# Kernel tuning notes

Measured on AMD Instinct MI355X. Metric: run time of the kernel, lower is better.

The kernel has to match this reference:

```python
import jax, jax.numpy as jnp
import numpy as np

N = 100000          # num nodes
NUM_GRAPHS = 64
NEG_SLOPE = 0.2     # PyG GATv2Conv default


def gatv2_layer(x, src, dst, Wl, bl, Wr, br, att, bias, heads, out_ch, concat):
    # x: [N, F_in]; src/dst: [E] (self-loops already included)
    xl = (x @ Wl + bl).reshape(-1, heads, out_ch)   # source transform
    xr = (x @ Wr + br).reshape(-1, heads, out_ch)   # target transform
    m = jax.nn.leaky_relu(xl[src] + xr[dst], NEG_SLOPE)      # [E, H, C]
    alpha = jnp.einsum('ehc,hc->eh', m, att)                 # [E, H]
    # segment softmax over destination nodes
    amax = jax.ops.segment_max(alpha, dst, num_segments=N)
    alpha = jnp.exp(alpha - amax[dst])
    denom = jax.ops.segment_sum(alpha, dst, num_segments=N)
    alpha = alpha / (denom[dst] + 1e-16)
    out = jax.ops.segment_sum(xl[src] * alpha[..., None], dst, num_segments=N)
    out = out.reshape(N, heads * out_ch) if concat else out.mean(axis=1)
    return out + bias


def setup_inputs() -> dict:
    key = jax.random.key(0)
    ks = jax.random.split(key, 16)
    E = 3200000
    x = jax.random.normal(ks[0], (N, 256), dtype=jnp.float32)
    edge_index = jax.random.randint(ks[1], (2, E), 0, N, dtype=jnp.int64)
    batch = jnp.sort(jax.random.randint(ks[2], (N,), 0, NUM_GRAPHS, dtype=jnp.int64))
    H1, C1 = 8, 4
    s1 = 1.0 / np.sqrt(256)
    s2 = 1.0 / np.sqrt(H1 * C1)
    return {
        'x': x, 'edge_index': edge_index, 'batch': batch,
        'W1l': jax.random.normal(ks[3], (256, H1 * C1), jnp.float32) * s1,
        'b1l': jnp.zeros((H1 * C1,), jnp.float32),
        'W1r': jax.random.normal(ks[4], (256, H1 * C1), jnp.float32) * s1,
        'b1r': jnp.zeros((H1 * C1,), jnp.float32),
        'att1': jax.random.normal(ks[5], (H1, C1), jnp.float32),
        'bias1': jnp.zeros((H1 * C1,), jnp.float32),
        'W2l': jax.random.normal(ks[6], (H1 * C1, 64), jnp.float32) * s2,
        'b2l': jnp.zeros((64,), jnp.float32),
        'W2r': jax.random.normal(ks[7], (H1 * C1, 64), jnp.float32) * s2,
        'b2r': jnp.zeros((64,), jnp.float32),
        'att2': jax.random.normal(ks[8], (1, 64), jnp.float32),
        'bias2': jnp.zeros((64,), jnp.float32),
    }


def reference(x, edge_index, batch, W1l, b1l, W1r, b1r, att1, bias1,
              W2l, b2l, W2r, b2r, att2, bias2):
    # add self-loops (PyG GATv2Conv default add_self_loops=True)
    loop = jnp.arange(N, dtype=edge_index.dtype)
    src = jnp.concatenate([edge_index[0], loop])
    dst = jnp.concatenate([edge_index[1], loop])
    h = gatv2_layer(x, src, dst, W1l, b1l, W1r, b1r, att1, bias1, 8, 4, True)
    h = jax.nn.elu(h)
    h = gatv2_layer(h, src, dst, W2l, b2l, W2r, b2r, att2, bias2, 1, 64, False)
    # global mean pool over graphs
    sums = jax.ops.segment_sum(h, batch, num_segments=NUM_GRAPHS)
    counts = jax.ops.segment_sum(jnp.ones((N, 1), h.dtype), batch, num_segments=NUM_GRAPHS)
    return sums / jnp.maximum(counts, 1.0)
```

## Files before the change

kernel.cpp:

```cpp
#include <hip/hip_runtime.h>
#include <math.h>

#define NN 100000
#define EE 3200000
#define ET (EE + NN)
#define NG 64

#define NB 196
#define BWID 512
#define PCHUNK 4096
#define PBLOCKS ((ET + PCHUNK - 1) / PCHUNK)
#define PART_SMEM (NB * 12 + 1024 + PCHUNK * 4 + PCHUNK)

#define X1_SPLIT 50048
#define X1BLK_A 391
#define X1BLK_B 391

#define OFF_XL1B  0u
#define OFF_XR1   1600000u
#define OFF_HL2B  8000000u
#define OFF_HR2   11200000u
#define OFF_BEDGE 8000000u
#define OFF_RP    17600000u
#define OFF_ESRC  17700096u
#define OFF_POOL  21000096u
#define OFF_CNTG  21004192u
#define OFF_BCNT  21004256u
#define OFF_BOFF  21004512u
#define OFF_GCUR  21004768u
#define OFF_AL2   21005024u
#define OFF_AR2   21105024u
#define WS_UNITS  21205024u

__device__ __forceinline__ float lrelu(float v) { return fmaxf(v, 0.2f * v); }

__device__ __forceinline__ unsigned pack_bf2(float a, float b) {
  unsigned ua = __float_as_uint(a), ub = __float_as_uint(b);
  ua = (ua + 0x7FFFu + ((ua >> 16) & 1u)) >> 16;
  ub = (ub + 0x7FFFu + ((ub >> 16) & 1u)) & 0xFFFF0000u;
  return ua | ub;
}
__device__ __forceinline__ float bf_lo(unsigned u) { return __uint_as_float(u << 16); }
__device__ __forceinline__ float bf_hi(unsigned u) { return __uint_as_float(u & 0xFFFF0000u); }

typedef float f32x2 __attribute__((ext_vector_type(2)));
__device__ __forceinline__ f32x2 pk_add(f32x2 a, f32x2 b) {
  f32x2 r; asm("v_pk_add_f32 %0, %1, %2" : "=v"(r) : "v"(a), "v"(b)); return r;
}
__device__ __forceinline__ f32x2 pk_mul(f32x2 a, f32x2 b) {
  f32x2 r; asm("v_pk_mul_f32 %0, %1, %2" : "=v"(r) : "v"(a), "v"(b)); return r;
}
__device__ __forceinline__ f32x2 pk_fma(f32x2 a, f32x2 b, f32x2 c) {
  f32x2 r; asm("v_pk_fma_f32 %0, %1, %2, %3" : "=v"(r) : "v"(a), "v"(b), "v"(c)); return r;
}
__device__ __forceinline__ f32x2 unpk2(unsigned u) {
  f32x2 r; r.x = __uint_as_float(u << 16); r.y = __uint_as_float(u & 0xFFFF0000u); return r;
}
__device__ __forceinline__ f32x2 abs2(f32x2 a) {
  f32x2 r;
  r.x = __uint_as_float(__float_as_uint(a.x) & 0x7FFFFFFFu);
  r.y = __uint_as_float(__float_as_uint(a.y) & 0x7FFFFFFFu);
  return r;
}

__global__ __launch_bounds__(256) void k_bcount(const int* __restrict__ ei,
                                                int* __restrict__ bcnt) {
  __shared__ int h[NB];
  for (int i = threadIdx.x; i < NB; i += 256) h[i] = 0;
  __syncthreads();
  for (long e = (long)blockIdx.x * 256 + threadIdx.x; e < ET; e += (long)gridDim.x * 256) {
    int d = (e < EE) ? ei[EE + e] : (int)(e - EE);
    atomicAdd(&h[d >> 9], 1);
  }
  __syncthreads();
  for (int i = threadIdx.x; i < NB; i += 256) if (h[i]) atomicAdd(&bcnt[i], h[i]);
}

__global__ __launch_bounds__(256) void k_bscan(const int* __restrict__ bcnt,
                                               int* __restrict__ boff, int* __restrict__ gcur) {
  __shared__ int sd[256];
  int t = threadIdx.x;
  int v = (t < NB) ? bcnt[t] : 0;
  sd[t] = v;
  __syncthreads();
  for (int o = 1; o < 256; o <<= 1) {
    int u = (t >= o) ? sd[t - o] : 0;
    __syncthreads();
    sd[t] += u;
    __syncthreads();
  }
  if (t < NB) { boff[t] = sd[t] - v; gcur[t] = sd[t] - v; }
  if (t == 0) boff[NB] = ET;
}

__device__ void part_role(char* smem, const int* __restrict__ ei,
                          int* __restrict__ gcur, int* __restrict__ bedge, int pblk) {
  int* cnt   = (int*)smem;
  int* lbase = cnt + NB;
  int* gbase = lbase + NB;
  int* sc    = gbase + NB;
  int* buf   = sc + 256;
  unsigned char* bkt = (unsigned char*)(buf + PCHUNK);
  int tid = threadIdx.x;
  long e0 = (long)pblk * PCHUNK;
  int nedge = (e0 + PCHUNK <= ET) ? PCHUNK : (int)(ET - e0);

  for (int i = tid; i < NB; i += 512) cnt[i] = 0;
  __syncthreads();
  for (int i = tid; i < nedge; i += 512) {
    long e = e0 + i;
    int d = (e < EE) ? ei[EE + e] : (int)(e - EE);
    atomicAdd(&cnt[d >> 9], 1);
  }
  __syncthreads();
  if (tid < 256) sc[tid] = (tid < NB) ? cnt[tid] : 0;
  __syncthreads();
  for (int o = 1; o < 256; o <<= 1) {
    int u = (tid < 256 && tid >= o) ? sc[tid - o] : 0;
    __syncthreads();
    if (tid < 256) sc[tid] += u;
    __syncthreads();
  }
  if (tid < NB) lbase[tid] = sc[tid] - cnt[tid];
  __syncthreads();
  if (tid < NB) {
    int c = cnt[tid];
    gbase[tid] = c ? atomicAdd(&gcur[tid], c) : 0;
    cnt[tid] = 0;
  }
  __syncthreads();
  for (int i = tid; i < nedge; i += 512) {
    long e = e0 + i;
    int s, d;
    if (e < EE) { s = ei[e]; d = ei[EE + e]; }
    else { s = (int)(e - EE); d = s; }
    int b = d >> 9;
    int r = atomicAdd(&cnt[b], 1);
    int idx = lbase[b] + r;
    buf[idx] = s | ((d & 511) << 17);
    bkt[idx] = (unsigned char)b;
  }
  __syncthreads();
  for (int i = tid; i < nedge; i += 512) {
    int p = buf[i];
    int b = bkt[i];
    bedge[gbase[b] + (i - lbase[b])] = p;
  }
}

__device__ void csr_role(char* smem, const int* __restrict__ boff,
                         const int* __restrict__ bedge,
                         int* __restrict__ rp, int* __restrict__ esrc, int b) {
  int* sdeg  = (int*)smem;
  int* sscan = sdeg + BWID;
  int t = threadIdx.x;
  int n0 = b * BWID;
  int lo = boff[b], hi = boff[b + 1];
  sdeg[t] = 0;
  __syncthreads();
  for (int i = lo + t; i < hi; i += 512) {
    int p = bedge[i];
    atomicAdd(&sdeg[p >> 17], 1);
  }
  __syncthreads();
  int v = sdeg[t];
  sscan[t] = v;
  __syncthreads();
  for (int o = 1; o < 512; o <<= 1) {
    int u = (t >= o) ? sscan[t - o] : 0;
    __syncthreads();
    sscan[t] += u;
    __syncthreads();
  }
  int excl = sscan[t] - v;
  int n = n0 + t;
  if (n < NN) rp[n] = lo + excl;
  if (b == NB - 1 && t == 0) rp[NN] = ET;
  __syncthreads();
  sdeg[t] = lo + excl;
  __syncthreads();
  for (int i = lo + t; i < hi; i += 512) {
    int p = bedge[i];
    int pos = atomicAdd(&sdeg[p >> 17], 1);
    esrc[pos] = p & 0x1FFFF;
  }
}

#define FMA4A(a, xv) \
  a.x += xv.x*w0.x + xv.y*w1.x + xv.z*w2.x + xv.w*w3.x; \
  a.y += xv.x*w0.y + xv.y*w1.y + xv.z*w2.y + xv.w*w3.y; \
  a.z += xv.x*w0.z + xv.y*w1.z + xv.z*w2.z + xv.w*w3.z; \
  a.w += xv.x*w0.w + xv.y*w1.w + xv.z*w2.w + xv.w*w3.w;

__device__ void xform1_role(char* smem, const float* __restrict__ x,
                            const float* __restrict__ Wl, const float* __restrict__ bl,
                            const float* __restrict__ Wr, const float* __restrict__ br,
                            unsigned short* __restrict__ xl1b, float* __restrict__ xr1,
                            int n_base) {
  float* Wlds = (float*)smem;
  int tid = threadIdx.x;
  int ci = tid & 15;
  int cbase = ci * 4;
  int n0 = n_base + (tid >> 4) * 4;
  int r0 = n0 + 0 < NN ? n0 + 0 : NN - 1;
  int r1 = n0 + 1 < NN ? n0 + 1 : NN - 1;
  int r2 = n0 + 2 < NN ? n0 + 2 : NN - 1;
  int r3 = n0 + 3 < NN ? n0 + 3 : NN - 1;
  const float* xb0 = x + (size_t)r0 * 256;
  const float* xb1 = x + (size_t)r1 * 256;
  const float* xb2 = x + (size_t)r2 * 256;
  const float* xb3 = x + (size_t)r3 * 256;
  float4 acc0 = {0,0,0,0}, acc1 = {0,0,0,0}, acc2 = {0,0,0,0}, acc3 = {0,0,0,0};

  for (int q = 0; q < 4; ++q) {
    int k0 = q * 64;
    __syncthreads();
    for (int i = tid; i < 64 * 64; i += 512) {
      int k = (i >> 6) + k0, c = i & 63;
      Wlds[i] = (c < 32) ? Wl[k * 32 + c] : Wr[k * 32 + (c - 32)];
    }
    __syncthreads();
#pragma unroll 2
    for (int kk = 0; kk < 64; kk += 4) {
      int k = k0 + kk;
      float4 xv0 = *(const float4*)(xb0 + k);
      float4 xv1 = *(const float4*)(xb1 + k);
      float4 xv2 = *(const float4*)(xb2 + k);
      float4 xv3 = *(const float4*)(xb3 + k);
      const float* wr = &Wlds[kk * 64 + cbase];
      float4 w0 = *(const float4*)(wr);
      float4 w1 = *(const float4*)(wr + 64);
      float4 w2 = *(const float4*)(wr + 128);
      float4 w3 = *(const float4*)(wr + 192);
      FMA4A(acc0, xv0)
      FMA4A(acc1, xv1)
      FMA4A(acc2, xv2)
      FMA4A(acc3, xv3)
    }
  }
  float4 acc[4] = {acc0, acc1, acc2, acc3};
  if (cbase < 32) {
    float4 bv = { bl[cbase], bl[cbase+1], bl[cbase+2], bl[cbase+3] };
#pragma unroll
    for (int j = 0; j < 4; ++j) {
      int n = n0 + j;
      if (n < NN) {
        uint2 o = { pack_bf2(acc[j].x + bv.x, acc[j].y + bv.y),
                    pack_bf2(acc[j].z + bv.z, acc[j].w + bv.w) };
        *(uint2*)(xl1b + (size_t)n * 32 + cbase) = o;
      }
    }
  } else {
    int c2 = cbase - 32;
    float4 bv = { br[c2], br[c2+1], br[c2+2], br[c2+3] };
#pragma unroll
    for (int j = 0; j < 4; ++j) {
      int n = n0 + j;
      if (n < NN) {
        float4 o = { acc[j].x + bv.x, acc[j].y + bv.y, acc[j].z + bv.z, acc[j].w + bv.w };
        *(float4*)(xr1 + (size_t)n * 32 + c2) = o;
      }
    }
  }
}

__global__ __launch_bounds__(512) void k_part_x1(
    const int* __restrict__ ei, int* __restrict__ gcur, int* __restrict__ bedge,
    const float* __restrict__ x,
    const float* __restrict__ Wl, const float* __restrict__ bl,
    const float* __restrict__ Wr, const float* __restrict__ br,
    unsigned short* __restrict__ xl1b, float* __restrict__ xr1) {
  extern __shared__ char smem[];
  if (blockIdx.x < PBLOCKS)
    part_role(smem, ei, gcur, bedge, blockIdx.x);
  else
    xform1_role(smem, x, Wl, bl, Wr, br, xl1b, xr1, (blockIdx.x - PBLOCKS) * 128);
}

__global__ __launch_bounds__(512) void k_csr_x1(
    const int* __restrict__ boff, const int* __restrict__ bedge,
    int* __restrict__ rp, int* __restrict__ esrc,
    const float* __restrict__ x,
    const float* __restrict__ Wl, const float* __restrict__ bl,
    const float* __restrict__ Wr, const float* __restrict__ br,
    unsigned short* __restrict__ xl1b, float* __restrict__ xr1) {
  extern __shared__ char smem[];
  if (blockIdx.x < NB)
    csr_role(smem, boff, bedge, rp, esrc, blockIdx.x);
  else
    xform1_role(smem, x, Wl, bl, Wr, br, xl1b, xr1,
                X1_SPLIT + (blockIdx.x - NB) * 128);
}

__global__ __launch_bounds__(256) void k_gather1x2(
    const int* __restrict__ rp, const int* __restrict__ esrc,
    const unsigned short* __restrict__ xl1b, const float* __restrict__ xr1,
    const float* __restrict__ att1, const float* __restrict__ bias1,
    const float* __restrict__ W2l, const float* __restrict__ b2l,
    const float* __restrict__ W2r, const float* __restrict__ b2r,
    const float* __restrict__ att2,
    unsigned short* __restrict__ hl2b, float* __restrict__ hr2,
    float* __restrict__ AL2, float* __restrict__ AR2) {
  __shared__ float W2lds[32 * 128];
  __shared__ float hlds[8][33];
  int tid = threadIdx.x;
  for (int i = tid; i < 32 * 128; i += 256) {
    int k = i >> 7, c = i & 127;
    W2lds[i] = (c < 64) ? W2l[k * 64 + c] : W2r[k * 64 + (c - 64)];
  }
  int n = blockIdx.x * 8 + (tid >> 5);
  int l = tid & 31;
  float av = att1[l];
  float xr = xr1[(size_t)n * 32 + l];
  int rpn = rp[n], dg = rp[n + 1] - rpn;
  float acc = 0.0f, den = 0.0f;
  int j = 0;
  for (; j + 4 <= dg; j += 4) {
    int s0 = esrc[rpn + j + 0];
    int s1 = esrc[rpn + j + 1];
    int s2 = esrc[rpn + j + 2];
    int s3 = esrc[rpn + j + 3];
    float x0 = bf_lo(xl1b[(size_t)s0 * 32 + l]);
    float x1 = bf_lo(xl1b[(size_t)s1 * 32 + l]);
    float x2 = bf_lo(xl1b[(size_t)s2 * 32 + l]);
    float x3 = bf_lo(xl1b[(size_t)s3 * 32 + l]);
    float p0 = lrelu(x0 + xr) * av;
    float p1 = lrelu(x1 + xr) * av;
    float p2 = lrelu(x2 + xr) * av;
    float p3 = lrelu(x3 + xr) * av;
    p0 += __shfl_xor(p0, 1); p1 += __shfl_xor(p1, 1);
    p2 += __shfl_xor(p2, 1); p3 += __shfl_xor(p3, 1);
    p0 += __shfl_xor(p0, 2); p1 += __shfl_xor(p1, 2);
    p2 += __shfl_xor(p2, 2); p3 += __shfl_xor(p3, 2);
    float w0 = __expf(p0), w1 = __expf(p1), w2 = __expf(p2), w3 = __expf(p3);
    den += w0 + w1 + w2 + w3;
    acc += w0 * x0 + w1 * x1 + w2 * x2 + w3 * x3;
  }
  for (; j < dg; ++j) {
    int s = esrc[rpn + j];
    float xl = bf_lo(xl1b[(size_t)s * 32 + l]);
    float p = lrelu(xl + xr) * av;
    p += __shfl_xor(p, 1);
    p += __shfl_xor(p, 2);
    float w = __expf(p);
    den += w;
    acc += w * xl;
  }
  float v = acc / (den + 1e-16f) + bias1[l];
  v = v > 0.0f ? v : expm1f(v);
  hlds[tid >> 5][l] = v;
  __syncthreads();

  int ni = tid >> 5, ci = tid & 31, cbase = ci * 4;
  float4 a = {0,0,0,0};
#pragma unroll
  for (int k = 0; k < 32; ++k) {
    float hv = hlds[ni][k];
    float4 wv = *(const float4*)(&W2lds[k * 128 + cbase]);
    a.x += hv * wv.x; a.y += hv * wv.y; a.z += hv * wv.z; a.w += hv * wv.w;
  }
  int no = blockIdx.x * 8 + ni;
  float partial;
  if (cbase < 64) {
    uint2 o = { pack_bf2(a.x + b2l[cbase], a.y + b2l[cbase + 1]),
                pack_bf2(a.z + b2l[cbase + 2], a.w + b2l[cbase + 3]) };
    *(uint2*)(hl2b + (size_t)no * 64 + cbase) = o;
    partial = bf_lo(o.x) * att2[cbase + 0] + bf_hi(o.x) * att2[cbase + 1]
            + bf_lo(o.y) * att2[cbase + 2] + bf_hi(o.y) * att2[cbase + 3];
  } else {
    int c2 = cbase - 64;
    float4 o = { a.x + b2r[c2], a.y + b2r[c2 + 1], a.z + b2r[c2 + 2], a.w + b2r[c2 + 3] };
    *(float4*)(hr2 + (size_t)no * 64 + c2) = o;
    partial = o.x * att2[c2 + 0] + o.y * att2[c2 + 1]
            + o.z * att2[c2 + 2] + o.w * att2[c2 + 3];
  }
  partial += __shfl_xor(partial, 1);
  partial += __shfl_xor(partial, 2);
  partial += __shfl_xor(partial, 4);
  partial += __shfl_xor(partial, 8);
  if (ci == 0)  AL2[no] = partial;
  if (ci == 16) AR2[no] = partial;
}

#define G2E(qq, u0O, u1O, u2O, u3O, pO) \
  f32x2 u0O = unpk2(qq.x), u1O = unpk2(qq.y), u2O = unpk2(qq.z), u3O = unpk2(qq.w); \
  float pO; { \
    f32x2 pa__ = pk_mul(abs2(pk_add(u0O, hp0)), ap0); \
    pa__ = pk_fma(abs2(pk_add(u1O, hp1)), ap1, pa__); \
    pa__ = pk_fma(abs2(pk_add(u2O, hp2)), ap2, pa__); \
    pa__ = pk_fma(abs2(pk_add(u3O, hp3)), ap3, pa__); \
    pO = pa__.x + pa__.y; }

#define G2A(u0O, u1O, u2O, u3O, ww) { \
  f32x2 wv__; wv__.x = (ww); wv__.y = (ww); \
  A0 = pk_fma(u0O, wv__, A0); A1 = pk_fma(u1O, wv__, A1); \
  A2 = pk_fma(u2O, wv__, A2); A3 = pk_fma(u3O, wv__, A3); }

__global__ __launch_bounds__(256) void k_gather2(
    const int* __restrict__ rp, const int* __restrict__ esrc,
    const unsigned short* __restrict__ hl2b, const float* __restrict__ hr2,
    const float* __restrict__ att2, const float* __restrict__ bias2,
    const int* __restrict__ batch,
    const float* __restrict__ AL2, const float* __restrict__ AR2,
    float* __restrict__ pool, float* __restrict__ cntg) {
  __shared__ float ssum[4][64];
  __shared__ float scnt[4];
  int tid = threadIdx.x;
  int n = (blockIdx.x * 256 + tid) >> 3;
  int l8 = tid & 7;
  int nblk0 = blockIdx.x * 32;
  int gmin = batch[nblk0];
  int gspan = batch[nblk0 + 31] - gmin + 1;
  ssum[tid >> 6][tid & 63] = 0.0f;
  if (tid < 4) scnt[tid] = 0.0f;
  __syncthreads();

  float4 ac0 = *(const float4*)(att2 + l8 * 8);
  float4 ac1 = *(const float4*)(att2 + l8 * 8 + 4);
  float4 bs0 = *(const float4*)(bias2 + l8 * 8);
  float4 bs1 = *(const float4*)(bias2 + l8 * 8 + 4);
  f32x2 ap0, ap1, ap2, ap3;
  ap0.x = ac0.x; ap0.y = ac0.y; ap1.x = ac0.z; ap1.y = ac0.w;
  ap2.x = ac1.x; ap2.y = ac1.y; ap3.x = ac1.z; ap3.y = ac1.w;
  const float4* hrp = (const float4*)(hr2 + (size_t)n * 64 + l8 * 8);
  float4 h0 = hrp[0], h1 = hrp[1];
  f32x2 hp0, hp1, hp2, hp3;
  hp0.x = h0.x; hp0.y = h0.y; hp1.x = h0.z; hp1.y = h0.w;
  hp2.x = h1.x; hp2.y = h1.y; hp3.x = h1.z; hp3.y = h1.w;
  float ard = 0.6f * AR2[n];
  int rpn = rp[n], dg = rp[n + 1] - rpn;
  f32x2 A0 = {0.f,0.f}, A1 = {0.f,0.f}, A2 = {0.f,0.f}, A3 = {0.f,0.f};
  float den = 0.0f;
  int j = 0;
  for (; j + 4 <= dg; j += 4) {
    int s0 = esrc[rpn + j + 0];
    int s1 = esrc[rpn + j + 1];
    int s2 = esrc[rpn + j + 2];
    int s3 = esrc[rpn + j + 3];
    uint4 q0 = *(const uint4*)(hl2b + (size_t)s0 * 64 + l8 * 8);
    uint4 q1 = *(const uint4*)(hl2b + (size_t)s1 * 64 + l8 * 8);
    uint4 q2 = *(const uint4*)(hl2b + (size_t)s2 * 64 + l8 * 8);
    uint4 q3 = *(const uint4*)(hl2b + (size_t)s3 * 64 + l8 * 8);
    float al0 = AL2[s0], al1 = AL2[s1], al2 = AL2[s2], al3 = AL2[s3];
    G2E(q0, e0u0, e0u1, e0u2, e0u3, p0)
    G2E(q1, e1u0, e1u1, e1u2, e1u3, p1)
    G2E(q2, e2u0, e2u1, e2u2, e2u3, p2)
    G2E(q3, e3u0, e3u1, e3u2, e3u3, p3)
    p0 += __shfl_xor(p0, 1); p1 += __shfl_xor(p1, 1);
    p2 += __shfl_xor(p2, 1); p3 += __shfl_xor(p3, 1);
    p0 += __shfl_xor(p0, 2); p1 += __shfl_xor(p1, 2);
    p2 += __shfl_xor(p2, 2); p3 += __shfl_xor(p3, 2);
    p0 += __shfl_xor(p0, 4); p1 += __shfl_xor(p1, 4);
    p2 += __shfl_xor(p2, 4); p3 += __shfl_xor(p3, 4);
    float w0 = __expf(fmaf(0.6f, al0, fmaf(0.4f, p0, ard)));
    float w1 = __expf(fmaf(0.6f, al1, fmaf(0.4f, p1, ard)));
    float w2 = __expf(fmaf(0.6f, al2, fmaf(0.4f, p2, ard)));
    float w3 = __expf(fmaf(0.6f, al3, fmaf(0.4f, p3, ard)));
    den += w0 + w1 + w2 + w3;
    G2A(e0u0, e0u1, e0u2, e0u3, w0)
    G2A(e1u0, e1u1, e1u2, e1u3, w1)
    G2A(e2u0, e2u1, e2u2, e2u3, w2)
    G2A(e3u0, e3u1, e3u2, e3u3, w3)
  }
  for (; j < dg; ++j) {
    int s = esrc[rpn + j];
    uint4 q0 = *(const uint4*)(hl2b + (size_t)s * 64 + l8 * 8);
    float al = AL2[s];
    G2E(q0, tu0, tu1, tu2, tu3, p)
    p += __shfl_xor(p, 1);
    p += __shfl_xor(p, 2);
    p += __shfl_xor(p, 4);
    float w = __expf(fmaf(0.6f, al, fmaf(0.4f, p, ard)));
    den += w;
    G2A(tu0, tu1, tu2, tu3, w)
  }
  float inv = 1.0f / (den + 1e-16f);
  int gi = batch[n] - gmin;
  float* sp = &ssum[gi][l8 * 8];
  atomicAdd(sp + 0, A0.x * inv + bs0.x);
  atomicAdd(sp + 1, A0.y * inv + bs0.y);
  atomicAdd(sp + 2, A1.x * inv + bs0.z);
  atomicAdd(sp + 3, A1.y * inv + bs0.w);
  atomicAdd(sp + 4, A2.x * inv + bs1.x);
  atomicAdd(sp + 5, A2.y * inv + bs1.y);
  atomicAdd(sp + 6, A3.x * inv + bs1.z);
  atomicAdd(sp + 7, A3.y * inv + bs1.w);
  if (l8 == 0) atomicAdd(&scnt[gi], 1.0f);
  __syncthreads();
  for (int i = tid; i < gspan * 64; i += 256)
    atomicAdd(pool + (size_t)(gmin + (i >> 6)) * 64 + (i & 63), ssum[i >> 6][i & 63]);
  if (tid < gspan) atomicAdd(cntg + gmin + tid, scnt[tid]);
}

__global__ __launch_bounds__(256) void k_final(
    const float* __restrict__ pool, const float* __restrict__ cntg,
    float* __restrict__ out) {
  int i = blockIdx.x * 256 + threadIdx.x;
  if (i < NG * 64) out[i] = pool[i] / fmaxf(cntg[i >> 6], 1.0f);
}

extern "C" void kernel_launch(void* const* d_in, const int* in_sizes, int n_in,
                              void* d_out, int out_size, void* d_ws, size_t ws_size,
                              hipStream_t stream) {
  const float* x     = (const float*)d_in[0];
  const int*   ei    = (const int*)d_in[1];
  const int*   batch = (const int*)d_in[2];
  const float* W1l   = (const float*)d_in[3];
  const float* b1l   = (const float*)d_in[4];
  const float* W1r   = (const float*)d_in[5];
  const float* b1r   = (const float*)d_in[6];
  const float* att1  = (const float*)d_in[7];
  const float* bias1 = (const float*)d_in[8];
  const float* W2l   = (const float*)d_in[9];
  const float* b2l   = (const float*)d_in[10];
  const float* W2r   = (const float*)d_in[11];
  const float* b2r   = (const float*)d_in[12];
  const float* att2  = (const float*)d_in[13];
  const float* bias2 = (const float*)d_in[14];
  float* ws = (float*)d_ws;
  int*   wi = (int*)d_ws;
  float* out = (float*)d_out;

  hipMemsetAsync(ws + OFF_POOL, 0, (size_t)(OFF_AL2 - OFF_POOL) * 4, stream);

  k_bcount<<<512, 256, 0, stream>>>(ei, wi + OFF_BCNT);
  k_bscan<<<1, 256, 0, stream>>>(wi + OFF_BCNT, wi + OFF_BOFF, wi + OFF_GCUR);
  k_part_x1<<<PBLOCKS + X1BLK_A, 512, PART_SMEM, stream>>>(
      ei, wi + OFF_GCUR, wi + OFF_BEDGE,
      x, W1l, b1l, W1r, b1r, (unsigned short*)(ws + OFF_XL1B), ws + OFF_XR1);
  k_csr_x1<<<NB + X1BLK_B, 512, 16384, stream>>>(
      wi + OFF_BOFF, wi + OFF_BEDGE, wi + OFF_RP, wi + OFF_ESRC,
      x, W1l, b1l, W1r, b1r, (unsigned short*)(ws + OFF_XL1B), ws + OFF_XR1);

  k_gather1x2<<<NN / 8, 256, 0, stream>>>(wi + OFF_RP, wi + OFF_ESRC,
                                          (const unsigned short*)(ws + OFF_XL1B), ws + OFF_XR1,
                                          att1, bias1, W2l, b2l, W2r, b2r, att2,
                                          (unsigned short*)(ws + OFF_HL2B), ws + OFF_HR2,
                                          ws + OFF_AL2, ws + OFF_AR2);
  k_gather2<<<(NN * 8 + 255) / 256, 256, 0, stream>>>(wi + OFF_RP, wi + OFF_ESRC,
                                                      (const unsigned short*)(ws + OFF_HL2B),
                                                      ws + OFF_HR2, att2, bias2, batch,
                                                      ws + OFF_AL2, ws + OFF_AR2,
                                                      ws + OFF_POOL, ws + OFF_CNTG);
  k_final<<<16, 256, 0, stream>>>(ws + OFF_POOL, ws + OFF_CNTG, out);
}
```

Measured before the change: 355.2 us.

## Restructure layer-1 gather to 8 lanes per node with packed bf16 loads

The layer-1 gather now assigns 8 lanes per destination node instead of 32. Each lane loads 4 bf16 channels (one head) as a uint2, so the per-head attention dot product needs no shuffle reduction. Leaky-relu is rewritten algebraically as 0.6*v + 0.4*|v| and evaluated with packed FMAs. Each block now handles 32 nodes and loops the fused layer-2 transform over 4 sub-batches, which amortises the W2 shared-memory fill over more nodes. The cost is fewer blocks and higher per-thread register use.

```diff
diff --git a/kernel.cpp b/kernel.cpp
--- a/kernel.cpp
+++ b/kernel.cpp
@@ -292,6 +292,16 @@
                 X1_SPLIT + (blockIdx.x - NB) * 128);
 }
 
+#define G1E(qq, u0O, u1O, pO) \
+  f32x2 u0O = unpk2(qq.x), u1O = unpk2(qq.y); \
+  float pO; { \
+    f32x2 v0__ = pk_add(u0O, xp0), v1__ = pk_add(u1O, xp1); \
+    f32x2 d__ = pk_mul(a6p0, v0__); \
+    d__ = pk_fma(a6p1, v1__, d__); \
+    d__ = pk_fma(a4p0, abs2(v0__), d__); \
+    d__ = pk_fma(a4p1, abs2(v1__), d__); \
+    pO = d__.x + d__.y; }
+
 __global__ __launch_bounds__(256) void k_gather1x2(
     const int* __restrict__ rp, const int* __restrict__ esrc,
     const unsigned short* __restrict__ xl1b, const float* __restrict__ xr1,
@@ -302,84 +312,111 @@
     unsigned short* __restrict__ hl2b, float* __restrict__ hr2,
     float* __restrict__ AL2, float* __restrict__ AR2) {
   __shared__ float W2lds[32 * 128];
-  __shared__ float hlds[8][33];
+  __shared__ float hlds[32][33];
   int tid = threadIdx.x;
   for (int i = tid; i < 32 * 128; i += 256) {
     int k = i >> 7, c = i & 127;
     W2lds[i] = (c < 64) ? W2l[k * 64 + c] : W2r[k * 64 + (c - 64)];
   }
-  int n = blockIdx.x * 8 + (tid >> 5);
-  int l = tid & 31;
-  float av = att1[l];
-  float xr = xr1[(size_t)n * 32 + l];
+  int nl = tid >> 3;
+  int n = blockIdx.x * 32 + nl;
+  int l8 = tid & 7;
+  float4 at = *(const float4*)(att1 + l8 * 4);
+  f32x2 a6p0, a6p1, a4p0, a4p1;
+  a6p0.x = 0.6f * at.x; a6p0.y = 0.6f * at.y;
+  a6p1.x = 0.6f * at.z; a6p1.y = 0.6f * at.w;
+  a4p0.x = 0.4f * at.x; a4p0.y = 0.4f * at.y;
+  a4p1.x = 0.4f * at.z; a4p1.y = 0.4f * at.w;
+  float4 xrv = *(const float4*)(xr1 + (size_t)n * 32 + l8 * 4);
+  f32x2 xp0, xp1;
+  xp0.x = xrv.x; xp0.y = xrv.y; xp1.x = xrv.z; xp1.y = xrv.w;
+
   int rpn = rp[n], dg = rp[n + 1] - rpn;
-  float acc = 0.0f, den = 0.0f;
+  f32x2 A0 = {0.f,0.f}, A1 = {0.f,0.f};
+  float den = 0.0f;
   int j = 0;
   for (; j + 4 <= dg; j += 4) {
     int s0 = esrc[rpn + j + 0];
     int s1 = esrc[rpn + j + 1];
     int s2 = esrc[rpn + j + 2];
     int s3 = esrc[rpn + j + 3];
-    float x0 = bf_lo(xl1b[(size_t)s0 * 32 + l]);
-    float x1 = bf_lo(xl1b[(size_t)s1 * 32 + l]);
-    float x2 = bf_lo(xl1b[(size_t)s2 * 32 + l]);
-    float x3 = bf_lo(xl1b[(size_t)s3 * 32 + l]);
-    float p0 = lrelu(x0 + xr) * av;
-    float p1 = lrelu(x1 + xr) * av;
-    float p2 = lrelu(x2 + xr) * av;
-    float p3 = lrelu(x3 + xr) * av;
-    p0 += __shfl_xor(p0, 1); p1 += __shfl_xor(p1, 1);
-    p2 += __shfl_xor(p2, 1); p3 += __shfl_xor(p3, 1);
-    p0 += __shfl_xor(p0, 2); p1 += __shfl_xor(p1, 2);
-    p2 += __shfl_xor(p2, 2); p3 += __shfl_xor(p3, 2);
+    uint2 q0 = *(const uint2*)(xl1b + (size_t)s0 * 32 + l8 * 4);
+    uint2 q1 = *(const uint2*)(xl1b + (size_t)s1 * 32 + l8 * 4);
+    uint2 q2 = *(const uint2*)(xl1b + (size_t)s2 * 32 + l8 * 4);
+    uint2 q3 = *(const uint2*)(xl1b + (size_t)s3 * 32 + l8 * 4);
+    G1E(q0, e0u0, e0u1, p0)
+    G1E(q1, e1u0, e1u1, p1)
+    G1E(q2, e2u0, e2u1, p2)
+    G1E(q3, e3u0, e3u1, p3)
     float w0 = __expf(p0), w1 = __expf(p1), w2 = __expf(p2), w3 = __expf(p3);
     den += w0 + w1 + w2 + w3;
-    acc += w0 * x0 + w1 * x1 + w2 * x2 + w3 * x3;
+    f32x2 wv0; wv0.x = w0; wv0.y = w0;
+    f32x2 wv1; wv1.x = w1; wv1.y = w1;
+    f32x2 wv2; wv2.x = w2; wv2.y = w2;
+    f32x2 wv3; wv3.x = w3; wv3.y = w3;
+    A0 = pk_fma(e0u0, wv0, A0); A1 = pk_fma(e0u1, wv0, A1);
+    A0 = pk_fma(e1u0, wv1, A0); A1 = pk_fma(e1u1, wv1, A1);
+    A0 = pk_fma(e2u0, wv2, A0); A1 = pk_fma(e2u1, wv2, A1);
+    A0 = pk_fma(e3u0, wv3, A0); A1 = pk_fma(e3u1, wv3, A1);
   }
   for (; j < dg; ++j) {
     int s = esrc[rpn + j];
-    float xl = bf_lo(xl1b[(size_t)s * 32 + l]);
-    float p = lrelu(xl + xr) * av;
-    p += __shfl_xor(p, 1);
-    p += __shfl_xor(p, 2);
+    uint2 q0 = *(const uint2*)(xl1b + (size_t)s * 32 + l8 * 4);
+    G1E(q0, tu0, tu1, p)
     float w = __expf(p);
     den += w;
-    acc += w * xl;
-  }
-  float v = acc / (den + 1e-16f) + bias1[l];
-  v = v > 0.0f ? v : expm1f(v);
-  hlds[tid >> 5][l] = v;
-  __syncthreads();
-
-  int ni = tid >> 5, ci = tid & 31, cbase = ci * 4;
-  float4 a = {0,0,0,0};
+    f32x2 wv; wv.x = w; wv.y = w;
+    A0 = pk_fma(tu0, wv, A0); A1 = pk_fma(tu1, wv, A1);
+  }
+  float inv = 1.0f / (den + 1e-16f);
+  float4 hb = *(const float4*)(bias1 + l8 * 4);
+  float h0 = A0.x * inv + hb.x;
+  float h1 = A0.y * inv + hb.y;
+  float h2 = A1.x * inv + hb.z;
+  float h3 = A1.y * inv + hb.w;
+  h0 = h0 > 0.0f ? h0 : expm1f(h0);
+  h1 = h1 > 0.0f ? h1 : expm1f(h1);
+  h2 = h2 > 0.0f ? h2 : expm1f(h2);
+  h3 = h3 > 0.0f ? h3 : expm1f(h3);
+  hlds[nl][l8 * 4 + 0] = h0;
+  hlds[nl][l8 * 4 + 1] = h1;
+  hlds[nl][l8 * 4 + 2] = h2;
+  hlds[nl][l8 * 4 + 3] = h3;
+  __syncthreads();
+
+  int ni8 = tid >> 5, ci = tid & 31, cbase = ci * 4;
 #pragma unroll
-  for (int k = 0; k < 32; ++k) {
-    float hv = hlds[ni][k];
-    float4 wv = *(const float4*)(&W2lds[k * 128 + cbase]);
-    a.x += hv * wv.x; a.y += hv * wv.y; a.z += hv * wv.z; a.w += hv * wv.w;
-  }
-  int no = blockIdx.x * 8 + ni;
-  float partial;
-  if (cbase < 64) {
-    uint2 o = { pack_bf2(a.x + b2l[cbase], a.y + b2l[cbase + 1]),
-                pack_bf2(a.z + b2l[cbase + 2], a.w + b2l[cbase + 3]) };
-    *(uint2*)(hl2b + (size_t)no * 64 + cbase) = o;
-    partial = bf_lo(o.x) * att2[cbase + 0] + bf_hi(o.x) * att2[cbase + 1]
-            + bf_lo(o.y) * att2[cbase + 2] + bf_hi(o.y) * att2[cbase + 3];
-  } else {
-    int c2 = cbase - 64;
-    float4 o = { a.x + b2r[c2], a.y + b2r[c2 + 1], a.z + b2r[c2 + 2], a.w + b2r[c2 + 3] };
-    *(float4*)(hr2 + (size_t)no * 64 + c2) = o;
-    partial = o.x * att2[c2 + 0] + o.y * att2[c2 + 1]
-            + o.z * att2[c2 + 2] + o.w * att2[c2 + 3];
-  }
-  partial += __shfl_xor(partial, 1);
-  partial += __shfl_xor(partial, 2);
-  partial += __shfl_xor(partial, 4);
-  partial += __shfl_xor(partial, 8);
-  if (ci == 0)  AL2[no] = partial;
-  if (ci == 16) AR2[no] = partial;
+  for (int sb = 0; sb < 4; ++sb) {
+    int nloc = sb * 8 + ni8;
+    float4 a = {0,0,0,0};
+#pragma unroll
+    for (int k = 0; k < 32; ++k) {
+      float hv = hlds[nloc][k];
+      float4 wv = *(const float4*)(&W2lds[k * 128 + cbase]);
+      a.x += hv * wv.x; a.y += hv * wv.y; a.z += hv * wv.z; a.w += hv * wv.w;
+    }
+    int no = blockIdx.x * 32 + nloc;
+    float partial;
+    if (cbase < 64) {
+      uint2 o = { pack_bf2(a.x + b2l[cbase], a.y + b2l[cbase + 1]),
+                  pack_bf2(a.z + b2l[cbase + 2], a.w + b2l[cbase + 3]) };
+      *(uint2*)(hl2b + (size_t)no * 64 + cbase) = o;
+      partial = bf_lo(o.x) * att2[cbase + 0] + bf_hi(o.x) * att2[cbase + 1]
+              + bf_lo(o.y) * att2[cbase + 2] + bf_hi(o.y) * att2[cbase + 3];
+    } else {
+      int c2 = cbase - 64;
+      float4 o = { a.x + b2r[c2], a.y + b2r[c2 + 1], a.z + b2r[c2 + 2], a.w + b2r[c2 + 3] };
+      *(float4*)(hr2 + (size_t)no * 64 + c2) = o;
+      partial = o.x * att2[c2 + 0] + o.y * att2[c2 + 1]
+              + o.z * att2[c2 + 2] + o.w * att2[c2 + 3];
+    }
+    partial += __shfl_xor(partial, 1);
+    partial += __shfl_xor(partial, 2);
+    partial += __shfl_xor(partial, 4);
+    partial += __shfl_xor(partial, 8);
+    if (ci == 0)  AL2[no] = partial;
+    if (ci == 16) AR2[no] = partial;
+  }
 }
 
 #define G2E(qq, u0O, u1O, u2O, u3O, pO) \
@@ -532,11 +569,11 @@
       wi + OFF_BOFF, wi + OFF_BEDGE, wi + OFF_RP, wi + OFF_ESRC,
       x, W1l, b1l, W1r, b1r, (unsigned short*)(ws + OFF_XL1B), ws + OFF_XR1);
 
-  k_gather1x2<<<NN / 8, 256, 0, stream>>>(wi + OFF_RP, wi + OFF_ESRC,
-                                          (const unsigned short*)(ws + OFF_XL1B), ws + OFF_XR1,
-                                          att1, bias1, W2l, b2l, W2r, b2r, att2,
-                                          (unsigned short*)(ws + OFF_HL2B), ws + OFF_HR2,
-                                          ws + OFF_AL2, ws + OFF_AR2);
+  k_gather1x2<<<NN / 32, 256, 0, stream>>>(wi + OFF_RP, wi + OFF_ESRC,
+                                           (const unsigned short*)(ws + OFF_XL1B), ws + OFF_XR1,
+                                           att1, bias1, W2l, b2l, W2r, b2r, att2,
+                                           (unsigned short*)(ws + OFF_HL2B), ws + OFF_HR2,
+                                           ws + OFF_AL2, ws + OFF_AR2);
   k_gather2<<<(NN * 8 + 255) / 256, 256, 0, stream>>>(wi + OFF_RP, wi + OFF_ESRC,
                                                       (const unsigned short*)(ws + OFF_HL2B),
                                                       ws + OFF_HR2, att2, bias2, batch,
```

Result: faster. 329.2 us (median of 3 runs) (-7.3%).
